# Kernel optimization log

Measured on AMD Instinct MI355X. Metric: run time of the kernel, lower is better.

Reference implementation:

```python
import jax, jax.numpy as jnp
import numpy as np

D_EMBED = 1024


def setup_inputs() -> dict:
    key = jax.random.key(0)
    ks = jax.random.split(key, 8)
    B, S, D = 8, 2048, D_EMBED
    scale = 1.0 / np.sqrt(D)
    return {
        "embeddings": jax.random.normal(ks[0], (B, S, D), dtype=jnp.float32),
        "mask": jnp.zeros((B, S, S), dtype=jnp.float32),
        "Wq": jax.random.normal(ks[1], (D, D), dtype=jnp.float32) * scale,
        "bq": jax.random.normal(ks[2], (D,), dtype=jnp.float32) * 0.02,
        "Wk": jax.random.normal(ks[3], (D, D), dtype=jnp.float32) * scale,
        "bk": jax.random.normal(ks[4], (D,), dtype=jnp.float32) * 0.02,
        "Wv": jax.random.normal(ks[5], (D, D), dtype=jnp.float32) * scale,
        "bv": jax.random.normal(ks[6], (D,), dtype=jnp.float32) * 0.02,
    }


def reference(embeddings, mask, Wq, bq, Wk, bk, Wv, bv):
    # torch Linear: y = x @ W.T + b
    q = jnp.einsum('bsd,ed->bse', embeddings, Wq) + bq
    k = jnp.einsum('bsd,ed->bse', embeddings, Wk) + bk
    v = jnp.einsum('bsd,ed->bse', embeddings, Wv) + bv
    scores = jnp.einsum('bqd,bkd->bqk', q, k)
    # NOTE: faithful to source — mask added BEFORE scaling by 1/sqrt(d)
    scores = (scores + mask) * (1.0 / jnp.sqrt(jnp.float32(q.shape[-1])))
    attn = jax.nn.softmax(scores, axis=-1)
    return jnp.einsum('bqk,bkd->bqd', attn, v)
```

## Files before the change

### kernel.cpp

```cpp
#include <hip/hip_runtime.h>


#define B_SZ 8
#define SEQ  2048
#define DIM  1024
#define MROWS (B_SZ * SEQ)

typedef unsigned short u16;
typedef short short8 __attribute__((ext_vector_type(8)));
typedef unsigned short u16x4 __attribute__((ext_vector_type(4)));
typedef float f32x4 __attribute__((ext_vector_type(4)));

__device__ __forceinline__ u16 f2h(float x) {
  _Float16 h = (_Float16)x;
  union { _Float16 f; u16 u; } c; c.f = h; return c.u;
}
__device__ __forceinline__ float h2f(u16 u) {
  union { _Float16 f; u16 u; } c; c.u = u; return (float)c.f;
}

__device__ __forceinline__ int xcd_swz(int x, int nwg) {
  return (x & 7) * (nwg >> 3) + (x >> 3);
}

__device__ __forceinline__ void gload_lds16(const u16* g, u16* l) {
  __builtin_amdgcn_global_load_lds(
      (__attribute__((address_space(1))) void*)(g),
      (__attribute__((address_space(3))) void*)(l), 16, 0, 0);
}

__device__ __forceinline__ f32x4 mfma_f16(short8 a, short8 b, f32x4 c) {
  asm("v_mfma_f32_16x16x32_f16 %0, %1, %2, %0" : "+v"(c) : "v"(a), "v"(b));
  return c;
}

__device__ __forceinline__ void gemm256_core(const u16* __restrict__ Ag,
                                             const u16* __restrict__ Bg,
                                             int NT, size_t lda, size_t ldb,
                                             u16* sm, f32x4 (&acc)[8][4]) {
  const int tid = threadIdx.x;
  const int lane = tid & 63;
  const int wid = tid >> 6;
  const int wm = wid >> 2;
  const int wn = wid & 3;
  const int wm8 = wm << 3;
  const int wn4 = wn << 2;

  u16* sA = sm;
  u16* sB = sm + 32768;

  const int bb = (lane << 4) ^ (((lane >> 5) & 1) << 5);
  const int rins = bb >> 6;
  const int cins = (bb & 63) >> 1;
  const int s0 = wid, s1 = 8 + wid, s2 = 16 + wid, s3 = 24 + wid;
  const size_t aoff0 = (size_t)((s0 >> 1) * 16 + rins) * lda + ((s0 & 1) * 32 + cins);
  const size_t aoff1 = (size_t)((s1 >> 1) * 16 + rins) * lda + ((s1 & 1) * 32 + cins);
  const size_t aoff2 = (size_t)((s2 >> 1) * 16 + rins) * lda + ((s2 & 1) * 32 + cins);
  const size_t aoff3 = (size_t)((s3 >> 1) * 16 + rins) * lda + ((s3 & 1) * 32 + cins);
  const size_t boff0 = (size_t)((s0 >> 1) * 16 + rins) * ldb + ((s0 & 1) * 32 + cins);
  const size_t boff1 = (size_t)((s1 >> 1) * 16 + rins) * ldb + ((s1 & 1) * 32 + cins);
  const size_t boff2 = (size_t)((s2 >> 1) * 16 + rins) * ldb + ((s2 & 1) * 32 + cins);
  const size_t boff3 = (size_t)((s3 >> 1) * 16 + rins) * ldb + ((s3 & 1) * 32 + cins);
  const int wid512 = wid << 9;

  const int lof = ((lane & 15) << 6) + ((lane >> 4) << 4);
  const int loe = (lof ^ (((lane >> 3) & 1) << 5)) >> 1;

#define ISSUE_A(j, nb, kt) \
  gload_lds16(Ag + aoff##j + (size_t)(kt) * 64, sA + (nb) * 16384 + (j) * 4096 + wid512)
#define ISSUE_B(j, nb, kt) \
  gload_lds16(Bg + boff##j + (size_t)(kt) * 64, sB + (nb) * 16384 + (j) * 4096 + wid512)

  ISSUE_B(0, 0, 0); ISSUE_B(1, 0, 0); ISSUE_B(2, 0, 0); ISSUE_B(3, 0, 0);
  ISSUE_A(0, 0, 0); ISSUE_A(1, 0, 0); ISSUE_A(2, 0, 0); ISSUE_A(3, 0, 0);

  int buf = 0;
  for (int kt = 0; kt < NT; ++kt) {
    const int nk = kt + 1;
    const bool pre = nk < NT;
    const int nb = buf ^ 1;
    asm volatile("s_waitcnt vmcnt(1)" ::: "memory");
    __builtin_amdgcn_s_barrier();
    asm volatile("" ::: "memory");
    const u16* bufA = sA + buf * 16384;
    const u16* bufB = sB + buf * 16384;
    short8 bf[4][2];
#pragma unroll
    for (int n = 0; n < 4; ++n) {
      bf[n][0] = *(const short8*)(bufB + (wn4 + n) * 1024 + loe);
      bf[n][1] = *(const short8*)(bufB + (wn4 + n) * 1024 + 512 + loe);
    }
    {
      short8 af[2][2];
#pragma unroll
      for (int m = 0; m < 2; ++m) {
        af[m][0] = *(const short8*)(bufA + (wm8 + m) * 1024 + loe);
        af[m][1] = *(const short8*)(bufA + (wm8 + m) * 1024 + 512 + loe);
      }
      if (pre) { ISSUE_B(0, nb, nk); ISSUE_B(1, nb, nk); }
      __builtin_amdgcn_s_setprio(1);
#pragma unroll
      for (int m = 0; m < 2; ++m)
#pragma unroll
        for (int n = 0; n < 4; ++n) {
          acc[m][n] = mfma_f16(af[m][0], bf[n][0], acc[m][n]);
          acc[m][n] = mfma_f16(af[m][1], bf[n][1], acc[m][n]);
        }
      __builtin_amdgcn_s_setprio(0);
    }
    {
      short8 af[2][2];
#pragma unroll
      for (int m = 0; m < 2; ++m) {
        af[m][0] = *(const short8*)(bufA + (wm8 + 2 + m) * 1024 + loe);
        af[m][1] = *(const short8*)(bufA + (wm8 + 2 + m) * 1024 + 512 + loe);
      }
      if (pre) { ISSUE_B(2, nb, nk); ISSUE_B(3, nb, nk); }
      __builtin_amdgcn_s_setprio(1);
#pragma unroll
      for (int m = 0; m < 2; ++m)
#pragma unroll
        for (int n = 0; n < 4; ++n) {
          acc[2 + m][n] = mfma_f16(af[m][0], bf[n][0], acc[2 + m][n]);
          acc[2 + m][n] = mfma_f16(af[m][1], bf[n][1], acc[2 + m][n]);
        }
      __builtin_amdgcn_s_setprio(0);
    }
    if (pre) {
      asm volatile("s_waitcnt vmcnt(4)" ::: "memory");
    } else {
      asm volatile("s_waitcnt vmcnt(0)" ::: "memory");
    }
    __builtin_amdgcn_s_barrier();
    asm volatile("" ::: "memory");
    {
      short8 af[2][2];
#pragma unroll
      for (int m = 0; m < 2; ++m) {
        af[m][0] = *(const short8*)(bufA + (wm8 + 4 + m) * 1024 + loe);
        af[m][1] = *(const short8*)(bufA + (wm8 + 4 + m) * 1024 + 512 + loe);
      }
      if (pre) { ISSUE_A(0, nb, nk); ISSUE_A(1, nb, nk); }
      __builtin_amdgcn_s_setprio(1);
#pragma unroll
      for (int m = 0; m < 2; ++m)
#pragma unroll
        for (int n = 0; n < 4; ++n) {
          acc[4 + m][n] = mfma_f16(af[m][0], bf[n][0], acc[4 + m][n]);
          acc[4 + m][n] = mfma_f16(af[m][1], bf[n][1], acc[4 + m][n]);
        }
      __builtin_amdgcn_s_setprio(0);
    }
    {
      short8 af[2][2];
#pragma unroll
      for (int m = 0; m < 2; ++m) {
        af[m][0] = *(const short8*)(bufA + (wm8 + 6 + m) * 1024 + loe);
        af[m][1] = *(const short8*)(bufA + (wm8 + 6 + m) * 1024 + 512 + loe);
      }
      if (pre) { ISSUE_A(2, nb, nk); ISSUE_A(3, nb, nk); }
      __builtin_amdgcn_s_setprio(1);
#pragma unroll
      for (int m = 0; m < 2; ++m)
#pragma unroll
        for (int n = 0; n < 4; ++n) {
          acc[6 + m][n] = mfma_f16(af[m][0], bf[n][0], acc[6 + m][n]);
          acc[6 + m][n] = mfma_f16(af[m][1], bf[n][1], acc[6 + m][n]);
        }
      __builtin_amdgcn_s_setprio(0);
    }
    buf ^= 1;
  }
  asm volatile("s_nop 7\n\ts_nop 7\n\ts_nop 7" ::);
#undef ISSUE_A
#undef ISSUE_B
}

__global__ __launch_bounds__(256) void cvt_kernel(const float* __restrict__ in,
                                                  u16* __restrict__ out, int n4) {
  int i = blockIdx.x * 256 + threadIdx.x;
  if (i >= n4) return;
  float4 v = ((const float4*)in)[i];
  u16x4 o;
  o[0] = f2h(v.x); o[1] = f2h(v.y); o[2] = f2h(v.z); o[3] = f2h(v.w);
  ((u16x4*)out)[i] = o;
}

__global__ __launch_bounds__(512) void proj256_kernel(const u16* __restrict__ emb16,
                                                      const u16* __restrict__ Bq,
                                                      const u16* __restrict__ Bk,
                                                      const u16* __restrict__ Bv,
                                                      const float* __restrict__ bq,
                                                      const float* __restrict__ bk,
                                                      const float* __restrict__ bv,
                                                      u16* __restrict__ q16,
                                                      u16* __restrict__ k16,
                                                      u16* __restrict__ vT) {
  __shared__ __align__(16) u16 sm[65536];
  const int wg = xcd_swz(blockIdx.x, 768);
  const int lane = threadIdx.x & 63, wid = threadIdx.x >> 6;
  f32x4 acc[8][4] = {};
  if (wg < 512) {
    const int m0 = (wg >> 3) * 256;
    const int z = (wg >> 2) & 1;
    const int n0 = (wg & 3) * 256;
    gemm256_core(emb16 + (size_t)m0 * 1024, (z ? Bk : Bq) + (size_t)n0 * 1024,
                 16, 1024, 1024, sm, acc);
    const int rb = m0 + ((wid >> 2) << 7) + ((lane >> 4) << 2);
    const int cb = n0 + ((wid & 3) << 6) + (lane & 15);
    const float* bias = z ? bk : bq;
    u16* dst = z ? k16 : q16;
#pragma unroll
    for (int m = 0; m < 8; ++m)
#pragma unroll
      for (int n = 0; n < 4; ++n)
#pragma unroll
        for (int j = 0; j < 4; ++j) {
          int row = rb + m * 16 + j;
          int col = cb + n * 16;
          dst[(size_t)row * DIM + col] = f2h(acc[m][n][j] + bias[col]);
        }
  } else {
    const int r = wg - 512;
    const int m0 = (r & 3) * 256;
    const int n0 = (r >> 2) * 256;
    gemm256_core(Bv + (size_t)m0 * 1024, emb16 + (size_t)n0 * 1024,
                 16, 1024, 1024, sm, acc);
    const int rb = m0 + ((wid >> 2) << 7) + ((lane >> 4) << 2);
    const int cb = n0 + ((wid & 3) << 6) + (lane & 15);
#pragma unroll
    for (int m = 0; m < 8; ++m)
#pragma unroll
      for (int n = 0; n < 4; ++n)
#pragma unroll
        for (int j = 0; j < 4; ++j) {
          int d = rb + m * 16 + j;
          int kg = cb + n * 16;
          int bi = kg >> 11, s = kg & 2047;
          vT[((size_t)bi << 21) + ((size_t)d << 11) + s] = f2h(acc[m][n][j] + bv[d]);
        }
  }
}

__global__ __launch_bounds__(512) void scores256_kernel(const u16* __restrict__ q16,
                                                        const u16* __restrict__ k16,
                                                        u16* __restrict__ scH) {
  __shared__ __align__(16) u16 sm[65536];
  const int wg = xcd_swz(blockIdx.x, 512);
  const int b = wg >> 6;
  const int m0 = ((wg >> 3) & 7) * 256;
  const int n0 = (wg & 7) * 256;
  f32x4 acc[8][4] = {};
  gemm256_core(q16 + ((size_t)b * SEQ + m0) * DIM, k16 + ((size_t)b * SEQ + n0) * DIM,
               16, DIM, DIM, sm, acc);
  const int lane = threadIdx.x & 63, wid = threadIdx.x >> 6;
  const int rb = m0 + ((wid >> 2) << 7) + ((lane >> 4) << 2);
  const int cb = n0 + ((wid & 3) << 6) + (lane & 15);
#pragma unroll
  for (int m = 0; m < 8; ++m)
#pragma unroll
    for (int n = 0; n < 4; ++n)
#pragma unroll
      for (int j = 0; j < 4; ++j) {
        size_t idx = ((size_t)b * SEQ + rb + m * 16 + j) * SEQ + (cb + n * 16);
        scH[idx] = f2h(acc[m][n][j] * 0.03125f);
      }
}

__global__ __launch_bounds__(256) void softmax_kernel(u16* __restrict__ scH,
                                                      const float* __restrict__ mask) {
  __shared__ float red[8];
  const size_t row = blockIdx.x;
  u16* rowp = scH + row * SEQ;
  const float* mrow = mask + row * SEQ;
  const int tid = threadIdx.x;
  short8 raw = *(const short8*)(rowp + tid * 8);
  float4 m0 = ((const float4*)mrow)[2 * tid];
  float4 m1 = ((const float4*)mrow)[2 * tid + 1];
  float mk[8] = {m0.x, m0.y, m0.z, m0.w, m1.x, m1.y, m1.z, m1.w};
  float f[8];
#pragma unroll
  for (int j = 0; j < 8; ++j) f[j] = h2f((u16)raw[j]) + mk[j] * 0.03125f;
  float mx = f[0];
#pragma unroll
  for (int j = 1; j < 8; ++j) mx = fmaxf(mx, f[j]);
#pragma unroll
  for (int off = 1; off < 64; off <<= 1) mx = fmaxf(mx, __shfl_xor(mx, off));
  const int wid = tid >> 6, lane = tid & 63;
  if (lane == 0) red[wid] = mx;
  __syncthreads();
  mx = fmaxf(fmaxf(red[0], red[1]), fmaxf(red[2], red[3]));
  float e[8];
  float s = 0.f;
#pragma unroll
  for (int j = 0; j < 8; ++j) {
    e[j] = __expf(f[j] - mx);
    s += e[j];
  }
#pragma unroll
  for (int off = 1; off < 64; off <<= 1) s += __shfl_xor(s, off);
  if (lane == 0) red[4 + wid] = s;
  __syncthreads();
  s = (red[4] + red[5]) + (red[6] + red[7]);
  const float inv = 1.f / s;
  short8 o;
#pragma unroll
  for (int j = 0; j < 8; ++j) o[j] = (short)f2h(e[j] * inv);
  *(short8*)(rowp + tid * 8) = o;
}

__global__ __launch_bounds__(512) void pv256_kernel(const u16* __restrict__ pr,
                                                    const u16* __restrict__ vt,
                                                    float* __restrict__ out) {
  __shared__ __align__(16) u16 sm[65536];
  const int wg = xcd_swz(blockIdx.x, 256);
  const int b = wg >> 5;
  const int m0 = ((wg >> 2) & 7) * 256;
  const int n0 = (wg & 3) * 256;
  f32x4 acc[8][4] = {};
  gemm256_core(pr + ((size_t)b * SEQ + m0) * SEQ, vt + ((size_t)b * DIM + n0) * SEQ,
               32, SEQ, SEQ, sm, acc);
  const int lane = threadIdx.x & 63, wid = threadIdx.x >> 6;
  const int rb = m0 + ((wid >> 2) << 7) + ((lane >> 4) << 2);
  const int cb = n0 + ((wid & 3) << 6) + (lane & 15);
#pragma unroll
  for (int m = 0; m < 8; ++m)
#pragma unroll
    for (int n = 0; n < 4; ++n)
#pragma unroll
      for (int j = 0; j < 4; ++j)
        out[((size_t)b * SEQ + rb + m * 16 + j) * DIM + (cb + n * 16)] = acc[m][n][j];
}

extern "C" void kernel_launch(void* const* d_in, const int* in_sizes, int n_in,
                              void* d_out, int out_size, void* d_ws, size_t ws_size,
                              hipStream_t stream) {
  const float* emb  = (const float*)d_in[0];
  const float* mask = (const float*)d_in[1];
  const float* Wq   = (const float*)d_in[2];
  const float* bq   = (const float*)d_in[3];
  const float* Wk   = (const float*)d_in[4];
  const float* bk   = (const float*)d_in[5];
  const float* Wv   = (const float*)d_in[6];
  const float* bv   = (const float*)d_in[7];
  float* out = (float*)d_out;

  const size_t M1 = 1024 * 1024;
  u16* scH   = (u16*)d_ws;
  u16* emb16 = scH + 32 * M1;
  u16* Bq  = emb16 + 16 * M1;
  u16* Bk  = Bq + 1 * M1;
  u16* Bv  = Bk + 1 * M1;
  u16* q16 = Bv + 1 * M1;
  u16* k16 = q16 + 16 * M1;
  u16* vT  = k16 + 16 * M1;

  cvt_kernel<<<16384, 256, 0, stream>>>(emb, emb16, (int)(4 * M1));
  cvt_kernel<<<1024, 256, 0, stream>>>(Wq, Bq, (int)(M1 / 4));
  cvt_kernel<<<1024, 256, 0, stream>>>(Wk, Bk, (int)(M1 / 4));
  cvt_kernel<<<1024, 256, 0, stream>>>(Wv, Bv, (int)(M1 / 4));

  proj256_kernel<<<768, 512, 0, stream>>>(emb16, Bq, Bk, Bv, bq, bk, bv, q16, k16, vT);

  scores256_kernel<<<512, 512, 0, stream>>>(q16, k16, scH);
  softmax_kernel<<<MROWS, 256, 0, stream>>>(scH, mask);
  pv256_kernel<<<256, 512, 0, stream>>>((const u16*)scH, vT, out);
}
```

Measured before the change: 305.8 us.

## Issue all next-tile prefetches early in GEMM loop and merge weight conversions

The GEMM core main loop now issues every global-to-LDS prefetch for the next K tile at the start of the first compute quarter, instead of spreading them over four quarters. The vmcnt waits change to match. The three weight fp32-to-fp16 conversion launches become one kernel that writes a contiguous B3 buffer, and proj256 indexes into it. The aim is more memory latency overlap and one less launch, at the cost of more outstanding loads and a burstier issue pattern. The vmcnt values must stay correct for the reordered A loads.

```diff
diff --git a/kernel.cpp b/kernel.cpp
--- a/kernel.cpp
+++ b/kernel.cpp
@@ -72,14 +72,14 @@
   gload_lds16(Bg + boff##j + (size_t)(kt) * 64, sB + (nb) * 16384 + (j) * 4096 + wid512)
 
   ISSUE_B(0, 0, 0); ISSUE_B(1, 0, 0); ISSUE_B(2, 0, 0); ISSUE_B(3, 0, 0);
-  ISSUE_A(0, 0, 0); ISSUE_A(1, 0, 0); ISSUE_A(2, 0, 0); ISSUE_A(3, 0, 0);
+  ISSUE_A(0, 0, 0); ISSUE_A(2, 0, 0); ISSUE_A(1, 0, 0); ISSUE_A(3, 0, 0);
 
   int buf = 0;
   for (int kt = 0; kt < NT; ++kt) {
     const int nk = kt + 1;
     const bool pre = nk < NT;
     const int nb = buf ^ 1;
-    asm volatile("s_waitcnt vmcnt(1)" ::: "memory");
+    asm volatile("s_waitcnt vmcnt(2)" ::: "memory");
     __builtin_amdgcn_s_barrier();
     asm volatile("" ::: "memory");
     const u16* bufA = sA + buf * 16384;
@@ -97,7 +97,10 @@
         af[m][0] = *(const short8*)(bufA + (wm8 + m) * 1024 + loe);
         af[m][1] = *(const short8*)(bufA + (wm8 + m) * 1024 + 512 + loe);
       }
-      if (pre) { ISSUE_B(0, nb, nk); ISSUE_B(1, nb, nk); }
+      if (pre) {
+        ISSUE_B(0, nb, nk); ISSUE_B(1, nb, nk); ISSUE_B(2, nb, nk); ISSUE_B(3, nb, nk);
+        ISSUE_A(0, nb, nk); ISSUE_A(2, nb, nk); ISSUE_A(1, nb, nk); ISSUE_A(3, nb, nk);
+      }
       __builtin_amdgcn_s_setprio(1);
 #pragma unroll
       for (int m = 0; m < 2; ++m)
@@ -115,7 +118,6 @@
         af[m][0] = *(const short8*)(bufA + (wm8 + 2 + m) * 1024 + loe);
         af[m][1] = *(const short8*)(bufA + (wm8 + 2 + m) * 1024 + 512 + loe);
       }
-      if (pre) { ISSUE_B(2, nb, nk); ISSUE_B(3, nb, nk); }
       __builtin_amdgcn_s_setprio(1);
 #pragma unroll
       for (int m = 0; m < 2; ++m)
@@ -127,7 +129,7 @@
       __builtin_amdgcn_s_setprio(0);
     }
     if (pre) {
-      asm volatile("s_waitcnt vmcnt(4)" ::: "memory");
+      asm volatile("s_waitcnt vmcnt(8)" ::: "memory");
     } else {
       asm volatile("s_waitcnt vmcnt(0)" ::: "memory");
     }
@@ -140,7 +142,6 @@
         af[m][0] = *(const short8*)(bufA + (wm8 + 4 + m) * 1024 + loe);
         af[m][1] = *(const short8*)(bufA + (wm8 + 4 + m) * 1024 + 512 + loe);
       }
-      if (pre) { ISSUE_A(0, nb, nk); ISSUE_A(1, nb, nk); }
       __builtin_amdgcn_s_setprio(1);
 #pragma unroll
       for (int m = 0; m < 2; ++m)
@@ -158,7 +159,6 @@
         af[m][0] = *(const short8*)(bufA + (wm8 + 6 + m) * 1024 + loe);
         af[m][1] = *(const short8*)(bufA + (wm8 + 6 + m) * 1024 + 512 + loe);
       }
-      if (pre) { ISSUE_A(2, nb, nk); ISSUE_A(3, nb, nk); }
       __builtin_amdgcn_s_setprio(1);
 #pragma unroll
       for (int m = 0; m < 2; ++m)
@@ -186,10 +186,22 @@
   ((u16x4*)out)[i] = o;
 }
 
+__global__ __launch_bounds__(256) void cvt_w3_kernel(const float* __restrict__ Wq,
+                                                     const float* __restrict__ Wk,
+                                                     const float* __restrict__ Wv,
+                                                     u16* __restrict__ B3) {
+  int b = blockIdx.x;
+  int w = b >> 10;
+  int i = (b & 1023) * 256 + threadIdx.x;
+  const float* src = (w == 0) ? Wq : (w == 1) ? Wk : Wv;
+  float4 v = ((const float4*)src)[i];
+  u16x4 o;
+  o[0] = f2h(v.x); o[1] = f2h(v.y); o[2] = f2h(v.z); o[3] = f2h(v.w);
+  ((u16x4*)(B3 + (size_t)w * DIM * DIM))[i] = o;
+}
+
 __global__ __launch_bounds__(512) void proj256_kernel(const u16* __restrict__ emb16,
-                                                      const u16* __restrict__ Bq,
-                                                      const u16* __restrict__ Bk,
-                                                      const u16* __restrict__ Bv,
+                                                      const u16* __restrict__ B3,
                                                       const float* __restrict__ bq,
                                                       const float* __restrict__ bk,
                                                       const float* __restrict__ bv,
@@ -204,7 +216,7 @@
     const int m0 = (wg >> 3) * 256;
     const int z = (wg >> 2) & 1;
     const int n0 = (wg & 3) * 256;
-    gemm256_core(emb16 + (size_t)m0 * 1024, (z ? Bk : Bq) + (size_t)n0 * 1024,
+    gemm256_core(emb16 + (size_t)m0 * 1024, B3 + (size_t)z * DIM * DIM + (size_t)n0 * 1024,
                  16, 1024, 1024, sm, acc);
     const int rb = m0 + ((wid >> 2) << 7) + ((lane >> 4) << 2);
     const int cb = n0 + ((wid & 3) << 6) + (lane & 15);
@@ -224,7 +236,7 @@
     const int r = wg - 512;
     const int m0 = (r & 3) * 256;
     const int n0 = (r >> 2) * 256;
-    gemm256_core(Bv + (size_t)m0 * 1024, emb16 + (size_t)n0 * 1024,
+    gemm256_core(B3 + (size_t)2 * DIM * DIM + (size_t)m0 * 1024, emb16 + (size_t)n0 * 1024,
                  16, 1024, 1024, sm, acc);
     const int rb = m0 + ((wid >> 2) << 7) + ((lane >> 4) << 2);
     const int cb = n0 + ((wid & 3) << 6) + (lane & 15);
@@ -348,19 +360,15 @@
   const size_t M1 = 1024 * 1024;
   u16* scH   = (u16*)d_ws;
   u16* emb16 = scH + 32 * M1;
-  u16* Bq  = emb16 + 16 * M1;
-  u16* Bk  = Bq + 1 * M1;
-  u16* Bv  = Bk + 1 * M1;
-  u16* q16 = Bv + 1 * M1;
+  u16* B3  = emb16 + 16 * M1;
+  u16* q16 = B3 + 3 * M1;
   u16* k16 = q16 + 16 * M1;
   u16* vT  = k16 + 16 * M1;
 
   cvt_kernel<<<16384, 256, 0, stream>>>(emb, emb16, (int)(4 * M1));
-  cvt_kernel<<<1024, 256, 0, stream>>>(Wq, Bq, (int)(M1 / 4));
-  cvt_kernel<<<1024, 256, 0, stream>>>(Wk, Bk, (int)(M1 / 4));
-  cvt_kernel<<<1024, 256, 0, stream>>>(Wv, Bv, (int)(M1 / 4));
-
-  proj256_kernel<<<768, 512, 0, stream>>>(emb16, Bq, Bk, Bv, bq, bk, bv, q16, k16, vT);
+  cvt_w3_kernel<<<3072, 256, 0, stream>>>(Wq, Wk, Wv, B3);
+
+  proj256_kernel<<<768, 512, 0, stream>>>(emb16, B3, bq, bk, bv, q16, k16, vT);
 
   scores256_kernel<<<512, 512, 0, stream>>>(q16, k16, scH);
   softmax_kernel<<<MROWS, 256, 0, stream>>>(scH, mask);
```

After: 312.0 us. 1.02x slower.
